# Optimization experiments

Hardware: AMD Instinct MI355X
Metric: run time of the kernel (lower is better)

## Reference

```python
import jax, jax.numpy as jnp
import numpy as np

# dims
B_, DM, DI, DS, DTR, DT_, G_, E_, K_, DC = 512, 1024, 2048, 64, 64, 64, 8, 4, 2, 4
# B_ batch, DM d_model, DI d_inner (expand*d_model), DS d_state, DTR dt_rank,
# DT_ D_time, G_ KAN grid size, E_ num_experts, K_ top_k, DC d_conv


def setup_inputs() -> dict:
    key = jax.random.key(0)
    ks = jax.random.split(key, 16)
    def n(i, shape, s=0.02):
        return jax.random.normal(ks[i], shape, dtype=jnp.float32) * s
    return {
        "uk_current_input": jax.random.normal(ks[0], (B_, DM), dtype=jnp.float32),
        "tk_current": jax.random.uniform(ks[1], (B_, 1), dtype=jnp.float32),
        "tk_previous": jax.random.uniform(ks[2], (B_, 1), dtype=jnp.float32),
        # input_proj
        "W_in": n(3, (DM, DM)), "b_in": jnp.zeros((DM,), jnp.float32),
        # K_MOTE router + sinusoidal time experts
        "router_W": n(4, (E_, 1), 1.0), "router_b": jnp.zeros((E_,), jnp.float32),
        "freq": jax.random.uniform(ks[5], (E_, DT_), minval=0.1, maxval=10.0),
        "phase": n(6, (E_, DT_), 1.0),
        "kan_W": n(7, (DT_, DT_, G_), 0.1),
        # Mamba SSM params
        "W_inproj": n(8, (2 * DI, DM)),
        "conv_w": n(9, (DI, DC), 0.1), "conv_b": jnp.zeros((DI,), jnp.float32),
        "W_x": n(10, (DTR + 2 * DS, DI)),
        "W_dt": n(11, (DI, DTR)), "dt_bias": jnp.full((DI,), -4.0, jnp.float32),
        "W_delta": n(12, (DI, DT_)),
        "A_log": jnp.log(jnp.tile(jnp.arange(1, DS + 1, dtype=jnp.float32), (DI, 1))),
        "D_skip": jnp.ones((DI,), jnp.float32),
        "W_out": n(13, (DM, DI)),
    }


def _k_mote(t, router_W, router_b, freq, phase):
    # t: (B,1) -> embedding (B, D_time), weights (B,E), mask (B,E)
    logits = t @ router_W.T + router_b                      # (B,E)
    w = jax.nn.softmax(logits, axis=-1)
    _, top_idx = jax.lax.top_k(w, K_)
    mask = jax.nn.one_hot(top_idx, E_, dtype=w.dtype).sum(axis=1)  # (B,E) binary
    w_sel = w * mask
    w_norm = w_sel / (w_sel.sum(axis=-1, keepdims=True) + 1e-8)
    # expert sinusoidal embeddings: (B,E,D_time)
    emb = jnp.sin(t[:, :, None] * freq[None] + phase[None])
    out = jnp.einsum('be,bed->bd', w_norm, emb)
    return out, w, mask


def _kan(x, kan_W):
    # rkhs_gaussian basis on fixed grid in [-1,1]
    grid = jnp.linspace(-1.0, 1.0, G_, dtype=x.dtype)
    h = 2.0 / (G_ - 1)
    phi = jnp.exp(-jnp.square((x[..., None] - grid) / h))   # (B, D_time, G)
    return jnp.einsum('big,oig->bo', phi, kan_W)


def _mamba_step(u, dt_emb, W_inproj, conv_w, conv_b, W_x, W_dt, dt_bias,
                W_delta, A_log, D_skip, W_out):
    # single-timestep selective scan (seq_len=1, zero initial state)
    xz = u @ W_inproj.T                                     # (B, 2*DI)
    x, z = jnp.split(xz, 2, axis=-1)
    # causal depthwise conv over a length-1 sequence with zero left-pad:
    # only the last kernel tap contributes
    x = x * conv_w[:, -1] + conv_b
    x = jax.nn.silu(x)
    x_dbl = x @ W_x.T                                       # (B, DTR+2*DS)
    dt_r = x_dbl[:, :DTR]
    Bmat = x_dbl[:, DTR:DTR + DS]                           # (B, DS)
    Cmat = x_dbl[:, DTR + DS:]                              # (B, DS)
    # dt modulated by the K-MOTE/KAN delta-time embedding
    dt = jax.nn.softplus(dt_r @ W_dt.T + dt_emb @ W_delta.T + dt_bias)  # (B, DI)
    # h_prev = 0 so exp(dt*A)*h_prev vanishes; h = (dt*B) * x
    h = (dt * x)[:, :, None] * Bmat[:, None, :]             # (B, DI, DS)
    y = jnp.einsum('bds,bs->bd', h, Cmat) + D_skip * x
    y = y * jax.nn.silu(z)
    return y @ W_out.T                                      # (B, DM)


def reference(uk_current_input, tk_current, tk_previous, W_in, b_in,
              router_W, router_b, freq, phase, kan_W, W_inproj, conv_w, conv_b,
              W_x, W_dt, dt_bias, W_delta, A_log, D_skip, W_out):
    processed_uk = uk_current_input @ W_in.T + b_in
    emb_tk, expert_weights, expert_mask = _k_mote(tk_current, router_W, router_b, freq, phase)
    emb_tk_prev, _, _ = _k_mote(tk_previous, router_W, router_b, freq, phase)
    delta_t_emb = _kan(emb_tk, kan_W) - _kan(emb_tk_prev, kan_W)
    hk = _mamba_step(processed_uk, delta_t_emb, W_inproj, conv_w, conv_b,
                     W_x, W_dt, dt_bias, W_delta, A_log, D_skip, W_out)
    return hk, expert_weights, expert_mask
```

## Files before the change

kernel.cpp:

```cpp
#include <hip/hip_runtime.h>
#include <hip/hip_bf16.h>
#include <math.h>

#define B_  512
#define DM  1024
#define DI  2048
#define DS  64
#define DTR 64
#define DT  64
#define G_  8
#define E_  4
#define DC  4

typedef __bf16 bf16x8 __attribute__((ext_vector_type(8)));
typedef float  f32x4  __attribute__((ext_vector_type(4)));
typedef unsigned short ushort_t;

__device__ __forceinline__ float bf2f(__hip_bfloat16 h) { return __bfloat162float(h); }
__device__ __forceinline__ __hip_bfloat16 f2bf(float f) { return __float2bfloat16(f); }
__device__ __forceinline__ float sigmoidf_(float x){ return 1.f/(1.f+expf(-x)); }
__device__ __forceinline__ float siluf_(float x){ return x*sigmoidf_(x); }
__device__ __forceinline__ float softplusf_(float x){ return (x>20.f)? x : log1pf(expf(x)); }

__device__ __forceinline__ unsigned int pack2(float a, float b) {
  unsigned short ua = __builtin_bit_cast(unsigned short, (__bf16)a);
  unsigned short ub = __builtin_bit_cast(unsigned short, (__bf16)b);
  return (unsigned int)ua | ((unsigned int)ub << 16);
}
__device__ __forceinline__ uint4 cvt8(float4 v0, float4 v1) {
  uint4 r;
  r.x = pack2(v0.x, v0.y); r.y = pack2(v0.z, v0.w);
  r.z = pack2(v1.x, v1.y); r.w = pack2(v1.z, v1.w);
  return r;
}

enum EpiKind { EPI_PART=0, EPI_G2=1, EPI_G4=2 };

struct EpiParams {
  const float* conv_w;
  const float* conv_b;
  __hip_bfloat16* xs;
  __hip_bfloat16* sz;
  const float* dt_bias;
  const float* dsk;
  const float* bc;
  __hip_bfloat16* yout;
  const float* b2;
};

template<int BM, int BN, int EK, bool CVTA, bool CVTB, bool B2>
__global__ __launch_bounds__(256)
void gemm_bt(const void* __restrict__ Ap, const void* __restrict__ Bp,
             void* __restrict__ Coutp, int Ka, int Kb, int kLen, int N,
             EpiParams ep)
{
  constexpr int BK = 64;
  constexpr int SA = 72;
  constexpr int NA = (BM*BK)/(256*8);
  constexpr int NB = (BN*BK)/(256*8);
  constexpr int WMT = (BM/2)/16;
  constexpr int WNT = (BN/2)/16;
  __shared__ ushort_t sA[2][BM*SA];
  __shared__ ushort_t sB[2][BN*SA];
  const int tid  = threadIdx.x;
  const int wave = tid >> 6, lane = tid & 63;
  const int wm = wave >> 1, wn = wave & 1;
  const int r = lane & 15, q = lane >> 4;
  const int bm = blockIdx.y * BM, bn = blockIdx.x * BN;
  const int kBase = blockIdx.z * kLen;
  const int T = kLen / BK;

  float4 fa[NA][2]; uint4 ua[NA];
  float4 fb[NB][2]; uint4 ub[NB];

  auto loadTiles = [&](int k0) {
    #pragma unroll
    for (int c=0;c<NA;++c) {
      int idx = tid*8 + c*2048; int row = idx>>6, kk = idx&63;
      if constexpr (CVTA) {
        const float* s = (const float*)Ap + (size_t)(bm+row)*Ka + k0 + kk;
        fa[c][0] = *reinterpret_cast<const float4*>(s);
        fa[c][1] = *reinterpret_cast<const float4*>(s+4);
      } else {
        const __hip_bfloat16* s = (const __hip_bfloat16*)Ap + (size_t)(bm+row)*Ka + k0 + kk;
        ua[c] = *reinterpret_cast<const uint4*>(s);
      }
    }
    #pragma unroll
    for (int c=0;c<NB;++c) {
      int idx = tid*8 + c*2048; int row = idx>>6, kk = idx&63;
      if constexpr (B2) {
        const float* bb = (k0==0) ? (const float*)Bp : ep.b2;
        const float* s = bb + (size_t)(bn+row)*Kb + kk;
        fb[c][0] = *reinterpret_cast<const float4*>(s);
        fb[c][1] = *reinterpret_cast<const float4*>(s+4);
      } else if constexpr (CVTB) {
        const float* s = (const float*)Bp + (size_t)(bn+row)*Kb + k0 + kk;
        fb[c][0] = *reinterpret_cast<const float4*>(s);
        fb[c][1] = *reinterpret_cast<const float4*>(s+4);
      } else {
        const __hip_bfloat16* s = (const __hip_bfloat16*)Bp + (size_t)(bn+row)*Kb + k0 + kk;
        ub[c] = *reinterpret_cast<const uint4*>(s);
      }
    }
  };
  auto writeTiles = [&](int buf) {
    #pragma unroll
    for (int c=0;c<NA;++c) {
      int idx = tid*8 + c*2048; int row = idx>>6, kk = idx&63;
      uint4 v; if constexpr (CVTA) v = cvt8(fa[c][0], fa[c][1]); else v = ua[c];
      *reinterpret_cast<uint4*>(&sA[buf][row*SA + kk]) = v;
    }
    #pragma unroll
    for (int c=0;c<NB;++c) {
      int idx = tid*8 + c*2048; int row = idx>>6, kk = idx&63;
      uint4 v; if constexpr (CVTB || B2) v = cvt8(fb[c][0], fb[c][1]); else v = ub[c];
      *reinterpret_cast<uint4*>(&sB[buf][row*SA + kk]) = v;
    }
  };

  f32x4 acc[WMT][WNT];
  #pragma unroll
  for (int i=0;i<WMT;++i)
    #pragma unroll
    for (int j=0;j<WNT;++j) acc[i][j] = (f32x4){0.f,0.f,0.f,0.f};

  loadTiles(kBase);
  writeTiles(0);
  for (int t=0; t<T; ++t) {
    __syncthreads();
    const int cur = t & 1;
    if (t+1 < T) loadTiles(kBase + (t+1)*BK);
    #pragma unroll
    for (int ks=0; ks<2; ++ks) {
      bf16x8 af[WMT], bfr[WNT];
      #pragma unroll
      for (int mt=0; mt<WMT; ++mt)
        af[mt] = *reinterpret_cast<const bf16x8*>(&sA[cur][(wm*(BM/2)+mt*16+r)*SA + ks*32 + q*8]);
      #pragma unroll
      for (int nt=0; nt<WNT; ++nt)
        bfr[nt] = *reinterpret_cast<const bf16x8*>(&sB[cur][(wn*(BN/2)+nt*16+r)*SA + ks*32 + q*8]);
      #pragma unroll
      for (int mt=0; mt<WMT; ++mt)
        #pragma unroll
        for (int nt=0; nt<WNT; ++nt)
          acc[mt][nt] = __builtin_amdgcn_mfma_f32_16x16x32_bf16(af[mt], bfr[nt], acc[mt][nt], 0,0,0);
    }
    if (t+1 < T) writeTiles(cur ^ 1);
  }

  #pragma unroll
  for (int mt=0; mt<WMT; ++mt) {
    #pragma unroll
    for (int nt=0; nt<WNT; ++nt) {
      #pragma unroll
      for (int i=0;i<4;++i) {
        int grow = bm + wm*(BM/2) + mt*16 + q*4 + i;
        int gcol = bn + wn*(BN/2) + nt*16 + r;
        float v = acc[mt][nt][i];
        if constexpr (EK == EPI_PART) {
          float* P = (float*)Coutp + (size_t)blockIdx.z * ((size_t)B_*N);
          P[(size_t)grow*N + gcol] = v;
        } else if constexpr (EK == EPI_G2) {
          if (gcol < DI) {
            float xc = v * ep.conv_w[gcol*DC + (DC-1)] + ep.conv_b[gcol];
            ep.xs[(size_t)grow*DI + gcol] = f2bf(siluf_(xc));
          } else {
            ep.sz[(size_t)grow*DI + (gcol - DI)] = f2bf(siluf_(v));
          }
        } else {
          float dt  = softplusf_(v + ep.dt_bias[gcol]);
          float xsv = bf2f(ep.xs[(size_t)grow*DI + gcol]);
          float szv = bf2f(ep.sz[(size_t)grow*DI + gcol]);
          float y = (dt * xsv * ep.bc[grow] + ep.dsk[gcol] * xsv) * szv;
          ep.yout[(size_t)grow*DI + gcol] = f2bf(y);
        }
      }
    }
  }
}


__global__ __launch_bounds__(256)
void reduce_bias_kernel(const float* __restrict__ part, const float* __restrict__ bias,
                        __hip_bfloat16* __restrict__ out)
{
  const int i = blockIdx.x*256 + threadIdx.x;
  const int total = B_*DM/4;
  const float4* p = (const float4*)part;
  float4 s = p[i];
  #pragma unroll
  for (int k=1;k<4;++k){ float4 t = p[i + k*total]; s.x+=t.x; s.y+=t.y; s.z+=t.z; s.w+=t.w; }
  float4 bv = ((const float4*)bias)[i & (DM/4 - 1)];
  uint2 o; o.x = pack2(s.x+bv.x, s.y+bv.y); o.y = pack2(s.z+bv.z, s.w+bv.w);
  ((uint2*)out)[i] = o;
}

__global__ __launch_bounds__(192)
void reduce_g3_kernel(const float* __restrict__ part, __hip_bfloat16* __restrict__ acat,
                      float* __restrict__ bc)
{
  const int row = blockIdx.x, col = threadIdx.x;
  const int stride = B_*192;
  float s = 0.f;
  #pragma unroll
  for (int k=0;k<8;++k) s += part[k*stride + row*192 + col];
  __shared__ float sBC[128];
  if (col < 64) acat[row*128 + col] = f2bf(s);
  else          sBC[col-64] = s;
  __syncthreads();
  if (col < 64) {
    float pval = sBC[col] * sBC[col+64];
    #pragma unroll
    for (int off=32; off; off>>=1) pval += __shfl_down(pval, off);
    if (col == 0) bc[row] = pval;
  }
}

__global__ __launch_bounds__(256)
void reduce_plain_kernel(const float* __restrict__ part, float* __restrict__ out)
{
  const int i = blockIdx.x*256 + threadIdx.x;
  const int total = B_*DM/4;
  const float4* p = (const float4*)part;
  float4 s = p[i];
  #pragma unroll
  for (int k=1;k<4;++k){ float4 t = p[i + k*total]; s.x+=t.x; s.y+=t.y; s.z+=t.z; s.w+=t.w; }
  ((float4*)out)[i] = s;
}


__device__ __forceinline__ void route(float t, const float* rW, const float* rb,
                                      float* w, float* mask, float* wn)
{
  float l[E_];
  float m = -1e30f;
  for (int e=0;e<E_;++e){ l[e] = t*rW[e] + rb[e]; m = fmaxf(m, l[e]); }
  float s = 0.f;
  for (int e=0;e<E_;++e){ w[e] = expf(l[e]-m); s += w[e]; }
  for (int e=0;e<E_;++e) w[e] /= s;
  int i1 = 0;
  for (int e=1;e<E_;++e) if (w[e] > w[i1]) i1 = e;
  int i2 = -1;
  for (int e=0;e<E_;++e) if (e != i1 && (i2 < 0 || w[e] > w[i2])) i2 = e;
  float ssel = w[i1] + w[i2] + 1e-8f;
  for (int e=0;e<E_;++e){
    float mk = (e==i1 || e==i2) ? 1.f : 0.f;
    mask[e] = mk;
    wn[e] = mk * w[e] / ssel;
  }
}

__global__ __launch_bounds__(64)
void mote_kan_kernel(const float* __restrict__ tk_c, const float* __restrict__ tk_p,
                     const float* __restrict__ rW, const float* __restrict__ rb,
                     const float* __restrict__ freq, const float* __restrict__ phase,
                     const float* __restrict__ kanW,
                     float* __restrict__ out_w, float* __restrict__ out_mask,
                     __hip_bfloat16* __restrict__ acat)
{
  const int b = blockIdx.x, tid = threadIdx.x;
  __shared__ float dphi[DT*G_];
  float t  = tk_c[b];
  float tp = tk_p[b];
  float w_c[E_], mask_c[E_], wn_c[E_];
  float w_p[E_], mask_p[E_], wn_p[E_];
  route(t,  rW, rb, w_c, mask_c, wn_c);
  route(tp, rW, rb, w_p, mask_p, wn_p);
  if (tid < E_) {
    out_w[b*E_ + tid]    = w_c[tid];
    out_mask[b*E_ + tid] = mask_c[tid];
  }
  float ec = 0.f, epv = 0.f;
  #pragma unroll
  for (int e=0;e<E_;++e) {
    float f  = freq[e*DT + tid];
    float ph = phase[e*DT + tid];
    ec  += wn_c[e] * sinf(t*f + ph);
    epv += wn_p[e] * sinf(tp*f + ph);
  }
  const float h = 2.f/(G_-1);
  #pragma unroll
  for (int g=0; g<G_; ++g) {
    float gr = -1.f + g*h;
    float a  = (ec - gr)/h;
    float bb = (epv - gr)/h;
    dphi[tid*G_ + g] = expf(-a*a) - expf(-bb*bb);
  }
  __syncthreads();
  float accv = 0.f;
  const float* kwrow = kanW + tid*DT*G_;
  for (int j=0;j<DT*G_;++j) accv += dphi[j] * kwrow[j];
  acat[b*128 + 64 + tid] = f2bf(accv);
}

extern "C" void kernel_launch(void* const* d_in, const int* in_sizes, int n_in,
                              void* d_out, int out_size, void* d_ws, size_t ws_size,
                              hipStream_t stream)
{
  const float* uk      = (const float*)d_in[0];
  const float* tk_c    = (const float*)d_in[1];
  const float* tk_p    = (const float*)d_in[2];
  const float* W_in    = (const float*)d_in[3];
  const float* b_in    = (const float*)d_in[4];
  const float* rW      = (const float*)d_in[5];
  const float* rb      = (const float*)d_in[6];
  const float* freq    = (const float*)d_in[7];
  const float* phase   = (const float*)d_in[8];
  const float* kanW    = (const float*)d_in[9];
  const float* W_inproj= (const float*)d_in[10];
  const float* conv_w  = (const float*)d_in[11];
  const float* conv_b  = (const float*)d_in[12];
  const float* W_x     = (const float*)d_in[13];
  const float* W_dt    = (const float*)d_in[14];
  const float* dt_bias = (const float*)d_in[15];
  const float* W_delta = (const float*)d_in[16];
  const float* D_skip  = (const float*)d_in[18];
  const float* W_out   = (const float*)d_in[19];

  char* ws = (char*)d_ws;
  __hip_bfloat16* Pu   = (__hip_bfloat16*)(ws);
  __hip_bfloat16* Xs   = (__hip_bfloat16*)(ws + (size_t)(1<<20));
  __hip_bfloat16* Sz   = (__hip_bfloat16*)(ws + (size_t)3*(1<<20));
  __hip_bfloat16* Yb   = (__hip_bfloat16*)(ws + (size_t)5*(1<<20));
  __hip_bfloat16* Acat = (__hip_bfloat16*)(ws + (size_t)7*(1<<20));
  float*          bc   = (float*)         (ws + (size_t)7*(1<<20) + (128<<10));
  float*          Part = (float*)         (ws + (size_t)8*(1<<20));

  float* out_hk   = (float*)d_out;
  float* out_w    = out_hk + (size_t)B_*DM;
  float* out_mask = out_w  + (size_t)B_*E_;

  mote_kan_kernel<<<dim3(B_), dim3(64), 0, stream>>>(tk_c, tk_p, rW, rb, freq, phase, kanW,
                                                     out_w, out_mask, Acat);

  { EpiParams p{};
    gemm_bt<32,64,EPI_PART,true,true,false><<<dim3(16,16,4), 256, 0, stream>>>(
        uk, W_in, Part, DM, DM, 256, DM, p); }
  reduce_bias_kernel<<<dim3(512), 256, 0, stream>>>(Part, b_in, Pu);

  { EpiParams p{}; p.conv_w = conv_w; p.conv_b = conv_b; p.xs = Xs; p.sz = Sz;
    gemm_bt<32,64,EPI_G2,false,true,false><<<dim3(64,16,1), 256, 0, stream>>>(
        Pu, W_inproj, nullptr, DM, DM, DM, 2*DI, p); }

  { EpiParams p{};
    gemm_bt<32,64,EPI_PART,false,true,false><<<dim3(3,16,8), 256, 0, stream>>>(
        Xs, W_x, Part, DI, DI, 256, 192, p); }
  reduce_g3_kernel<<<dim3(512), 192, 0, stream>>>(Part, Acat, bc);

  { EpiParams p{}; p.dt_bias = dt_bias; p.dsk = D_skip; p.bc = bc; p.xs = Xs; p.sz = Sz;
    p.yout = Yb; p.b2 = W_delta;
    gemm_bt<32,64,EPI_G4,false,true,true><<<dim3(32,16,1), 256, 0, stream>>>(
        Acat, W_dt, nullptr, 128, 64, 128, DI, p); }

  { EpiParams p{};
    gemm_bt<32,64,EPI_PART,false,true,false><<<dim3(16,16,4), 256, 0, stream>>>(
        Yb, W_out, Part, DI, DI, 512, DM, p); }
  reduce_plain_kernel<<<dim3(512), 256, 0, stream>>>(Part, out_hk);
}
```

Measured before the change: 183.5 us.

## Fuse all stages into one cooperative persistent kernel with grid syncs

Replaces the chain of separate kernel launches with a single cooperative kernel of 512 workgroups that runs every GEMM and reduction stage, separated by grid-wide syncs. The split-K partial buffers and reduce kernels for the input and output projections are dropped in favour of full-K tiles with BM=64 and epilogues that write directly, and the KAN job is packed four batch rows per workgroup. The aim is to remove launch gaps and the extra partial-sum traffic. In exchange it adds grid-sync costs, uses fewer and longer tiles for the first and last GEMMs, and keeps a fallback multi-kernel path in case the cooperative launch fails.

```diff
diff --git a/kernel.cpp b/kernel.cpp
--- a/kernel.cpp
+++ b/kernel.cpp
@@ -1,4 +1,5 @@
 #include <hip/hip_runtime.h>
+#include <hip/hip_cooperative_groups.h>
 #include <hip/hip_bf16.h>
 #include <math.h>
 
@@ -12,6 +13,8 @@
 #define E_  4
 #define DC  4
 
+namespace cg = cooperative_groups;
+
 typedef __bf16 bf16x8 __attribute__((ext_vector_type(8)));
 typedef float  f32x4  __attribute__((ext_vector_type(4)));
 typedef unsigned short ushort_t;
@@ -34,40 +37,33 @@
   return r;
 }
 
-enum EpiKind { EPI_PART=0, EPI_G2=1, EPI_G4=2 };
-
-struct EpiParams {
-  const float* conv_w;
-  const float* conv_b;
-  __hip_bfloat16* xs;
-  __hip_bfloat16* sz;
-  const float* dt_bias;
-  const float* dsk;
-  const float* bc;
-  __hip_bfloat16* yout;
-  const float* b2;
+enum EpiKind { EPI_PART=0, EPI_G2=1, EPI_G4=2, EPI_BIAS=3 };
+
+struct KParams {
+  const float *uk, *tk_c, *tk_p, *W_in, *b_in, *rW, *rb, *freq, *phase, *kanW;
+  const float *W_inproj, *conv_w, *conv_b, *W_x, *W_dt, *dt_bias, *W_delta, *D_skip, *W_out;
+  __hip_bfloat16 *Pu, *Xs, *Sz, *Yb, *Acat;
+  float *bc, *Part, *out_hk, *out_w, *out_mask;
 };
 
-template<int BM, int BN, int EK, bool CVTA, bool CVTB, bool B2>
-__global__ __launch_bounds__(256)
-void gemm_bt(const void* __restrict__ Ap, const void* __restrict__ Bp,
-             void* __restrict__ Coutp, int Ka, int Kb, int kLen, int N,
-             EpiParams ep)
-{
-  constexpr int BK = 64;
-  constexpr int SA = 72;
+template<int BM, int EK, bool CVTA, bool CVTB, bool B2>
+__device__ __forceinline__ void gemm_tile(char* smemc, int bxi, int byi, int bzi,
+    const void* __restrict__ Ap, const void* __restrict__ Bp, void* __restrict__ Coutp,
+    int Ka, int Kb, int kLen, int N, const KParams& p)
+{
+  constexpr int BN = 64, BK = 64, SA = 72;
   constexpr int NA = (BM*BK)/(256*8);
   constexpr int NB = (BN*BK)/(256*8);
   constexpr int WMT = (BM/2)/16;
   constexpr int WNT = (BN/2)/16;
-  __shared__ ushort_t sA[2][BM*SA];
-  __shared__ ushort_t sB[2][BN*SA];
+  ushort_t* sA = (ushort_t*)smemc;
+  ushort_t* sB = (ushort_t*)(smemc + (size_t)2*BM*SA*sizeof(ushort_t));
   const int tid  = threadIdx.x;
   const int wave = tid >> 6, lane = tid & 63;
   const int wm = wave >> 1, wn = wave & 1;
   const int r = lane & 15, q = lane >> 4;
-  const int bm = blockIdx.y * BM, bn = blockIdx.x * BN;
-  const int kBase = blockIdx.z * kLen;
+  const int bm = byi * BM, bn = bxi * BN;
+  const int kBase = bzi * kLen;
   const int T = kLen / BK;
 
   float4 fa[NA][2]; uint4 ua[NA];
@@ -90,7 +86,7 @@
     for (int c=0;c<NB;++c) {
       int idx = tid*8 + c*2048; int row = idx>>6, kk = idx&63;
       if constexpr (B2) {
-        const float* bb = (k0==0) ? (const float*)Bp : ep.b2;
+        const float* bb = (k0==0) ? (const float*)Bp : p.W_delta;
         const float* s = bb + (size_t)(bn+row)*Kb + kk;
         fb[c][0] = *reinterpret_cast<const float4*>(s);
         fb[c][1] = *reinterpret_cast<const float4*>(s+4);
@@ -109,13 +105,13 @@
     for (int c=0;c<NA;++c) {
       int idx = tid*8 + c*2048; int row = idx>>6, kk = idx&63;
       uint4 v; if constexpr (CVTA) v = cvt8(fa[c][0], fa[c][1]); else v = ua[c];
-      *reinterpret_cast<uint4*>(&sA[buf][row*SA + kk]) = v;
+      *reinterpret_cast<uint4*>(&sA[buf*(BM*SA) + row*SA + kk]) = v;
     }
     #pragma unroll
     for (int c=0;c<NB;++c) {
       int idx = tid*8 + c*2048; int row = idx>>6, kk = idx&63;
       uint4 v; if constexpr (CVTB || B2) v = cvt8(fb[c][0], fb[c][1]); else v = ub[c];
-      *reinterpret_cast<uint4*>(&sB[buf][row*SA + kk]) = v;
+      *reinterpret_cast<uint4*>(&sB[buf*(BN*SA) + row*SA + kk]) = v;
     }
   };
 
@@ -125,6 +121,7 @@
     #pragma unroll
     for (int j=0;j<WNT;++j) acc[i][j] = (f32x4){0.f,0.f,0.f,0.f};
 
+  __syncthreads();
   loadTiles(kBase);
   writeTiles(0);
   for (int t=0; t<T; ++t) {
@@ -136,10 +133,10 @@
       bf16x8 af[WMT], bfr[WNT];
       #pragma unroll
       for (int mt=0; mt<WMT; ++mt)
-        af[mt] = *reinterpret_cast<const bf16x8*>(&sA[cur][(wm*(BM/2)+mt*16+r)*SA + ks*32 + q*8]);
+        af[mt] = *reinterpret_cast<const bf16x8*>(&sA[cur*(BM*SA) + (wm*(BM/2)+mt*16+r)*SA + ks*32 + q*8]);
       #pragma unroll
       for (int nt=0; nt<WNT; ++nt)
-        bfr[nt] = *reinterpret_cast<const bf16x8*>(&sB[cur][(wn*(BN/2)+nt*16+r)*SA + ks*32 + q*8]);
+        bfr[nt] = *reinterpret_cast<const bf16x8*>(&sB[cur*(BN*SA) + (wn*(BN/2)+nt*16+r)*SA + ks*32 + q*8]);
       #pragma unroll
       for (int mt=0; mt<WMT; ++mt)
         #pragma unroll
@@ -159,74 +156,27 @@
         int gcol = bn + wn*(BN/2) + nt*16 + r;
         float v = acc[mt][nt][i];
         if constexpr (EK == EPI_PART) {
-          float* P = (float*)Coutp + (size_t)blockIdx.z * ((size_t)B_*N);
+          float* P = (float*)Coutp + (size_t)bzi * ((size_t)B_*N);
           P[(size_t)grow*N + gcol] = v;
+        } else if constexpr (EK == EPI_BIAS) {
+          p.Pu[(size_t)grow*N + gcol] = f2bf(v + p.b_in[gcol]);
         } else if constexpr (EK == EPI_G2) {
           if (gcol < DI) {
-            float xc = v * ep.conv_w[gcol*DC + (DC-1)] + ep.conv_b[gcol];
-            ep.xs[(size_t)grow*DI + gcol] = f2bf(siluf_(xc));
+            float xc = v * p.conv_w[gcol*DC + (DC-1)] + p.conv_b[gcol];
+            p.Xs[(size_t)grow*DI + gcol] = f2bf(siluf_(xc));
           } else {
-            ep.sz[(size_t)grow*DI + (gcol - DI)] = f2bf(siluf_(v));
+            p.Sz[(size_t)grow*DI + (gcol - DI)] = f2bf(siluf_(v));
           }
         } else {
-          float dt  = softplusf_(v + ep.dt_bias[gcol]);
-          float xsv = bf2f(ep.xs[(size_t)grow*DI + gcol]);
-          float szv = bf2f(ep.sz[(size_t)grow*DI + gcol]);
-          float y = (dt * xsv * ep.bc[grow] + ep.dsk[gcol] * xsv) * szv;
-          ep.yout[(size_t)grow*DI + gcol] = f2bf(y);
+          float dt  = softplusf_(v + p.dt_bias[gcol]);
+          float xsv = bf2f(p.Xs[(size_t)grow*DI + gcol]);
+          float szv = bf2f(p.Sz[(size_t)grow*DI + gcol]);
+          float y = (dt * xsv * p.bc[grow] + p.D_skip[gcol] * xsv) * szv;
+          p.Yb[(size_t)grow*DI + gcol] = f2bf(y);
         }
       }
     }
   }
-}
-
-
-__global__ __launch_bounds__(256)
-void reduce_bias_kernel(const float* __restrict__ part, const float* __restrict__ bias,
-                        __hip_bfloat16* __restrict__ out)
-{
-  const int i = blockIdx.x*256 + threadIdx.x;
-  const int total = B_*DM/4;
-  const float4* p = (const float4*)part;
-  float4 s = p[i];
-  #pragma unroll
-  for (int k=1;k<4;++k){ float4 t = p[i + k*total]; s.x+=t.x; s.y+=t.y; s.z+=t.z; s.w+=t.w; }
-  float4 bv = ((const float4*)bias)[i & (DM/4 - 1)];
-  uint2 o; o.x = pack2(s.x+bv.x, s.y+bv.y); o.y = pack2(s.z+bv.z, s.w+bv.w);
-  ((uint2*)out)[i] = o;
-}
-
-__global__ __launch_bounds__(192)
-void reduce_g3_kernel(const float* __restrict__ part, __hip_bfloat16* __restrict__ acat,
-                      float* __restrict__ bc)
-{
-  const int row = blockIdx.x, col = threadIdx.x;
-  const int stride = B_*192;
-  float s = 0.f;
-  #pragma unroll
-  for (int k=0;k<8;++k) s += part[k*stride + row*192 + col];
-  __shared__ float sBC[128];
-  if (col < 64) acat[row*128 + col] = f2bf(s);
-  else          sBC[col-64] = s;
-  __syncthreads();
-  if (col < 64) {
-    float pval = sBC[col] * sBC[col+64];
-    #pragma unroll
-    for (int off=32; off; off>>=1) pval += __shfl_down(pval, off);
-    if (col == 0) bc[row] = pval;
-  }
-}
-
-__global__ __launch_bounds__(256)
-void reduce_plain_kernel(const float* __restrict__ part, float* __restrict__ out)
-{
-  const int i = blockIdx.x*256 + threadIdx.x;
-  const int total = B_*DM/4;
-  const float4* p = (const float4*)part;
-  float4 s = p[i];
-  #pragma unroll
-  for (int k=1;k<4;++k){ float4 t = p[i + k*total]; s.x+=t.x; s.y+=t.y; s.z+=t.z; s.w+=t.w; }
-  ((float4*)out)[i] = s;
 }
 
 
@@ -251,110 +201,193 @@
   }
 }
 
-__global__ __launch_bounds__(64)
-void mote_kan_kernel(const float* __restrict__ tk_c, const float* __restrict__ tk_p,
-                     const float* __restrict__ rW, const float* __restrict__ rb,
-                     const float* __restrict__ freq, const float* __restrict__ phase,
-                     const float* __restrict__ kanW,
-                     float* __restrict__ out_w, float* __restrict__ out_mask,
-                     __hip_bfloat16* __restrict__ acat)
-{
-  const int b = blockIdx.x, tid = threadIdx.x;
-  __shared__ float dphi[DT*G_];
-  float t  = tk_c[b];
-  float tp = tk_p[b];
-  float w_c[E_], mask_c[E_], wn_c[E_];
-  float w_p[E_], mask_p[E_], wn_p[E_];
-  route(t,  rW, rb, w_c, mask_c, wn_c);
-  route(tp, rW, rb, w_p, mask_p, wn_p);
-  if (tid < E_) {
-    out_w[b*E_ + tid]    = w_c[tid];
-    out_mask[b*E_ + tid] = mask_c[tid];
-  }
-  float ec = 0.f, epv = 0.f;
-  #pragma unroll
-  for (int e=0;e<E_;++e) {
-    float f  = freq[e*DT + tid];
-    float ph = phase[e*DT + tid];
-    ec  += wn_c[e] * sinf(t*f + ph);
-    epv += wn_p[e] * sinf(tp*f + ph);
-  }
-  const float h = 2.f/(G_-1);
-  #pragma unroll
-  for (int g=0; g<G_; ++g) {
-    float gr = -1.f + g*h;
-    float a  = (ec - gr)/h;
-    float bb = (epv - gr)/h;
-    dphi[tid*G_ + g] = expf(-a*a) - expf(-bb*bb);
-  }
-  __syncthreads();
-  float accv = 0.f;
-  const float* kwrow = kanW + tid*DT*G_;
-  for (int j=0;j<DT*G_;++j) accv += dphi[j] * kwrow[j];
-  acat[b*128 + 64 + tid] = f2bf(accv);
+__device__ __forceinline__ void kan_job(char* smemc, int job, const KParams& p)
+{
+  float* dphi = (float*)smemc;
+  const int wv = threadIdx.x >> 6, lane = threadIdx.x & 63;
+  const int b = job*4 + wv;
+  __syncthreads();
+  {
+    float t  = p.tk_c[b];
+    float tp = p.tk_p[b];
+    float w_c[E_], mk_c[E_], wn_c[E_];
+    float w_p[E_], mk_p[E_], wn_p[E_];
+    route(t,  p.rW, p.rb, w_c, mk_c, wn_c);
+    route(tp, p.rW, p.rb, w_p, mk_p, wn_p);
+    if (lane < E_) {
+      p.out_w[b*E_ + lane]    = w_c[lane];
+      p.out_mask[b*E_ + lane] = mk_c[lane];
+    }
+    float ec = 0.f, epv = 0.f;
+    #pragma unroll
+    for (int e=0;e<E_;++e) {
+      float f  = p.freq[e*DT + lane];
+      float ph = p.phase[e*DT + lane];
+      ec  += wn_c[e] * sinf(t*f + ph);
+      epv += wn_p[e] * sinf(tp*f + ph);
+    }
+    const float h = 2.f/(G_-1);
+    #pragma unroll
+    for (int g=0; g<G_; ++g) {
+      float gr = -1.f + g*h;
+      float a  = (ec - gr)/h;
+      float bb = (epv - gr)/h;
+      dphi[wv*512 + lane*G_ + g] = expf(-a*a) - expf(-bb*bb);
+    }
+  }
+  __syncthreads();
+  {
+    float accv = 0.f;
+    const float* kw = p.kanW + (size_t)lane*(DT*G_);
+    const float* dd = dphi + wv*512;
+    #pragma unroll 4
+    for (int j=0;j<DT*G_;j+=4) {
+      float4 kv = *reinterpret_cast<const float4*>(kw + j);
+      float4 dv = *reinterpret_cast<const float4*>(dd + j);
+      accv += kv.x*dv.x + kv.y*dv.y + kv.z*dv.z + kv.w*dv.w;
+    }
+    p.Acat[b*128 + 64 + lane] = f2bf(accv);
+  }
+}
+
+__device__ __forceinline__ void r3_job(char* smemc, int row, const KParams& p)
+{
+  float* sbc = (float*)smemc;
+  const int col = threadIdx.x;
+  __syncthreads();
+  float s = 0.f;
+  if (col < 192) {
+    #pragma unroll
+    for (int k=0;k<8;++k) s += p.Part[(size_t)k*((size_t)B_*192) + row*192 + col];
+    if (col < 64) p.Acat[row*128 + col] = f2bf(s);
+    else          sbc[col-64] = s;
+  }
+  __syncthreads();
+  if (col < 64) {
+    float pval = sbc[col] * sbc[col+64];
+    #pragma unroll
+    for (int off=32; off; off>>=1) pval += __shfl_down(pval, off);
+    if (col == 0) p.bc[row] = pval;
+  }
+}
+
+__global__ __launch_bounds__(256, 2)
+void mega_kernel(KParams p)
+{
+  __shared__ __align__(16) char smem[2*64*72*2 + 2*64*72*2];
+  cg::grid_group grid = cg::this_grid();
+  const int wg = blockIdx.x;
+
+  if (wg < 128) {
+    gemm_tile<64,EPI_BIAS,true,true,false>(smem, wg&15, wg>>4, 0,
+        p.uk, p.W_in, nullptr, DM, DM, DM, DM, p);
+  } else if (wg < 256) {
+    kan_job(smem, wg-128, p);
+  }
+  grid.sync();
+
+  gemm_tile<64,EPI_G2,false,true,false>(smem, wg&63, wg>>6, 0,
+      p.Pu, p.W_inproj, nullptr, DM, DM, DM, 2*DI, p);
+  grid.sync();
+
+  if (wg < 384) {
+    const int bx = wg % 3, rem = wg / 3;
+    gemm_tile<32,EPI_PART,false,true,false>(smem, bx, rem&15, rem>>4,
+        p.Xs, p.W_x, p.Part, DI, DI, 256, 192, p);
+  }
+  grid.sync();
+
+  r3_job(smem, wg, p);
+  grid.sync();
+
+  gemm_tile<32,EPI_G4,false,true,true>(smem, wg&31, wg>>5, 0,
+      p.Acat, p.W_dt, nullptr, 128, 64, 128, DI, p);
+  grid.sync();
+
+  if (wg < 128) {
+    gemm_tile<64,EPI_PART,false,true,false>(smem, wg&15, wg>>4, 0,
+        p.Yb, p.W_out, p.out_hk, DI, DI, DI, DM, p);
+  }
+}
+
+
+template<int BM, int EK, bool CVTA, bool CVTB, bool B2>
+__global__ __launch_bounds__(256)
+void gemm_wrap(const void* __restrict__ Ap, const void* __restrict__ Bp,
+               void* __restrict__ Coutp, int Ka, int Kb, int kLen, int N, KParams p)
+{
+  __shared__ __align__(16) char smem[2*64*72*2 + 2*64*72*2];
+  gemm_tile<BM,EK,CVTA,CVTB,B2>(smem, blockIdx.x, blockIdx.y, blockIdx.z,
+                                Ap, Bp, Coutp, Ka, Kb, kLen, N, p);
+}
+
+__global__ __launch_bounds__(256)
+void kan_wrap(KParams p)
+{
+  __shared__ __align__(16) char smem[8192];
+  kan_job(smem, blockIdx.x, p);
+}
+
+__global__ __launch_bounds__(256)
+void r3_wrap(KParams p)
+{
+  __shared__ __align__(16) char smem[512];
+  r3_job(smem, blockIdx.x, p);
 }
 
 extern "C" void kernel_launch(void* const* d_in, const int* in_sizes, int n_in,
                               void* d_out, int out_size, void* d_ws, size_t ws_size,
                               hipStream_t stream)
 {
-  const float* uk      = (const float*)d_in[0];
-  const float* tk_c    = (const float*)d_in[1];
-  const float* tk_p    = (const float*)d_in[2];
-  const float* W_in    = (const float*)d_in[3];
-  const float* b_in    = (const float*)d_in[4];
-  const float* rW      = (const float*)d_in[5];
-  const float* rb      = (const float*)d_in[6];
-  const float* freq    = (const float*)d_in[7];
-  const float* phase   = (const float*)d_in[8];
-  const float* kanW    = (const float*)d_in[9];
-  const float* W_inproj= (const float*)d_in[10];
-  const float* conv_w  = (const float*)d_in[11];
-  const float* conv_b  = (const float*)d_in[12];
-  const float* W_x     = (const float*)d_in[13];
-  const float* W_dt    = (const float*)d_in[14];
-  const float* dt_bias = (const float*)d_in[15];
-  const float* W_delta = (const float*)d_in[16];
-  const float* D_skip  = (const float*)d_in[18];
-  const float* W_out   = (const float*)d_in[19];
+  KParams p;
+  p.uk       = (const float*)d_in[0];
+  p.tk_c     = (const float*)d_in[1];
+  p.tk_p     = (const float*)d_in[2];
+  p.W_in     = (const float*)d_in[3];
+  p.b_in     = (const float*)d_in[4];
+  p.rW       = (const float*)d_in[5];
+  p.rb       = (const float*)d_in[6];
+  p.freq     = (const float*)d_in[7];
+  p.phase    = (const float*)d_in[8];
+  p.kanW     = (const float*)d_in[9];
+  p.W_inproj = (const float*)d_in[10];
+  p.conv_w   = (const float*)d_in[11];
+  p.conv_b   = (const float*)d_in[12];
+  p.W_x      = (const float*)d_in[13];
+  p.W_dt     = (const float*)d_in[14];
+  p.dt_bias  = (const float*)d_in[15];
+  p.W_delta  = (const float*)d_in[16];
+  p.D_skip   = (const float*)d_in[18];
+  p.W_out    = (const float*)d_in[19];
 
   char* ws = (char*)d_ws;
-  __hip_bfloat16* Pu   = (__hip_bfloat16*)(ws);
-  __hip_bfloat16* Xs   = (__hip_bfloat16*)(ws + (size_t)(1<<20));
-  __hip_bfloat16* Sz   = (__hip_bfloat16*)(ws + (size_t)3*(1<<20));
-  __hip_bfloat16* Yb   = (__hip_bfloat16*)(ws + (size_t)5*(1<<20));
-  __hip_bfloat16* Acat = (__hip_bfloat16*)(ws + (size_t)7*(1<<20));
-  float*          bc   = (float*)         (ws + (size_t)7*(1<<20) + (128<<10));
-  float*          Part = (float*)         (ws + (size_t)8*(1<<20));
-
-  float* out_hk   = (float*)d_out;
-  float* out_w    = out_hk + (size_t)B_*DM;
-  float* out_mask = out_w  + (size_t)B_*E_;
-
-  mote_kan_kernel<<<dim3(B_), dim3(64), 0, stream>>>(tk_c, tk_p, rW, rb, freq, phase, kanW,
-                                                     out_w, out_mask, Acat);
-
-  { EpiParams p{};
-    gemm_bt<32,64,EPI_PART,true,true,false><<<dim3(16,16,4), 256, 0, stream>>>(
-        uk, W_in, Part, DM, DM, 256, DM, p); }
-  reduce_bias_kernel<<<dim3(512), 256, 0, stream>>>(Part, b_in, Pu);
-
-  { EpiParams p{}; p.conv_w = conv_w; p.conv_b = conv_b; p.xs = Xs; p.sz = Sz;
-    gemm_bt<32,64,EPI_G2,false,true,false><<<dim3(64,16,1), 256, 0, stream>>>(
-        Pu, W_inproj, nullptr, DM, DM, DM, 2*DI, p); }
-
-  { EpiParams p{};
-    gemm_bt<32,64,EPI_PART,false,true,false><<<dim3(3,16,8), 256, 0, stream>>>(
-        Xs, W_x, Part, DI, DI, 256, 192, p); }
-  reduce_g3_kernel<<<dim3(512), 192, 0, stream>>>(Part, Acat, bc);
-
-  { EpiParams p{}; p.dt_bias = dt_bias; p.dsk = D_skip; p.bc = bc; p.xs = Xs; p.sz = Sz;
-    p.yout = Yb; p.b2 = W_delta;
-    gemm_bt<32,64,EPI_G4,false,true,true><<<dim3(32,16,1), 256, 0, stream>>>(
-        Acat, W_dt, nullptr, 128, 64, 128, DI, p); }
-
-  { EpiParams p{};
-    gemm_bt<32,64,EPI_PART,false,true,false><<<dim3(16,16,4), 256, 0, stream>>>(
-        Yb, W_out, Part, DI, DI, 512, DM, p); }
-  reduce_plain_kernel<<<dim3(512), 256, 0, stream>>>(Part, out_hk);
-}
+  p.Pu   = (__hip_bfloat16*)(ws);
+  p.Xs   = (__hip_bfloat16*)(ws + (size_t)(1<<20));
+  p.Sz   = (__hip_bfloat16*)(ws + (size_t)3*(1<<20));
+  p.Yb   = (__hip_bfloat16*)(ws + (size_t)5*(1<<20));
+  p.Acat = (__hip_bfloat16*)(ws + (size_t)7*(1<<20));
+  p.bc   = (float*)         (ws + (size_t)7*(1<<20) + (128<<10));
+  p.Part = (float*)         (ws + (size_t)8*(1<<20));
+
+  p.out_hk   = (float*)d_out;
+  p.out_w    = p.out_hk + (size_t)B_*DM;
+  p.out_mask = p.out_w  + (size_t)B_*E_;
+
+  void* kargs[] = { &p };
+  hipError_t st = hipLaunchCooperativeKernel((void*)mega_kernel,
+                                             dim3(512), dim3(256), kargs, 0, stream);
+  if (st != hipSuccess) {
+    kan_wrap<<<dim3(128), 256, 0, stream>>>(p);
+    gemm_wrap<64,EPI_BIAS,true,true,false><<<dim3(16,8), 256, 0, stream>>>(
+        p.uk, p.W_in, nullptr, DM, DM, DM, DM, p);
+    gemm_wrap<64,EPI_G2,false,true,false><<<dim3(64,8), 256, 0, stream>>>(
+        p.Pu, p.W_inproj, nullptr, DM, DM, DM, 2*DI, p);
+    gemm_wrap<32,EPI_PART,false,true,false><<<dim3(3,16,8), 256, 0, stream>>>(
+        p.Xs, p.W_x, p.Part, DI, DI, 256, 192, p);
+    r3_wrap<<<dim3(512), 256, 0, stream>>>(p);
+    gemm_wrap<32,EPI_G4,false,true,true><<<dim3(32,16), 256, 0, stream>>>(
+        p.Acat, p.W_dt, nullptr, 128, 64, 128, DI, p);
+    gemm_wrap<64,EPI_PART,false,true,false><<<dim3(16,8), 256, 0, stream>>>(
+        p.Yb, p.W_out, p.out_hk, DI, DI, DI, DM, p);
+  }
+}
```

Result: slower. 489.6 us (+166.8%).
